# Kernel tuning notes

Measured on AMD Instinct MI355X. Metric: run time of the kernel, lower is better.

Reference implementation:

```python
import jax, jax.numpy as jnp
import numpy as np

B, T, D = 32, 2048, 1024
E, P, L = 16, 720, 8
TOP_K = 2
INIT_STD = 0.02


def _sdpa_1head(q, k, v):
    # q: [B,Q,D], k/v: [B,K,D]
    d = q.shape[-1]
    attn = jnp.einsum('bqd,bkd->bqk', q, k) / jnp.sqrt(jnp.asarray(d, q.dtype))
    attn = jax.nn.softmax(attn, axis=-1)
    return jnp.einsum('bqk,bkd->bqd', attn, v)


def setup_inputs() -> dict:
    key = jax.random.key(0)
    ks = jax.random.split(key, 18)
    s = INIT_STD
    def w(k, shape, scale=INIT_STD):
        return jax.random.normal(k, shape, jnp.float32) * scale
    return {
        'ctx_embed': jax.random.normal(ks[0], (B, T, D), jnp.float32),
        'query_experts': w(ks[1], (E, P, D)),
        'query_pos': w(ks[2], (P, D)),
        'pred_len_table': w(ks[3], (P + 1, D)),
        'latents': w(ks[4], (L, D)),
        'lat_q_w': w(ks[5], (D, D)),
        'ctx_k_w': w(ks[6], (D, D)),
        'ctx_v_w': w(ks[7], (D, D)),
        'lat_out_w': w(ks[8], (D, D)),
        'step_q_w': w(ks[9], (D, D)),
        'lat_k_w': w(ks[10], (D, D)),
        'lat_v_w': w(ks[11], (D, D)),
        'step_out_w': w(ks[12], (D, D)),
        'gate_w1': w(ks[13], (2 * D, D)),
        'gate_b1': jnp.zeros((D,), jnp.float32),
        'gate_w2': w(ks[14], (D, E)),
        'gate_b2': jnp.zeros((E,), jnp.float32),
        'pred_len': P,
    }


def reference(ctx_embed, query_experts, query_pos, pred_len_table, latents,
              lat_q_w, ctx_k_w, ctx_v_w, lat_out_w,
              step_q_w, lat_k_w, lat_v_w, step_out_w,
              gate_w1, gate_b1, gate_w2, gate_b2, pred_len):
    b, _, d = ctx_embed.shape
    # step base: positional + pred-len embedding
    pos = query_pos[:pred_len][None]                      # [1,P,D]
    len_vec = pred_len_table[pred_len][None, None, :]     # [1,1,D]
    step_base = jnp.broadcast_to(pos + len_vec, (b, pred_len, d))
    # stage 1: latents attend over context
    lat = jnp.broadcast_to(latents[None], (b,) + latents.shape)
    q1 = lat @ lat_q_w
    k1 = ctx_embed @ ctx_k_w
    v1 = ctx_embed @ ctx_v_w
    lat_ctx = _sdpa_1head(q1, k1, v1) @ lat_out_w         # [B,L,D]
    # stage 2: steps attend over latents
    q2 = step_base @ step_q_w
    k2 = lat_ctx @ lat_k_w
    v2 = lat_ctx @ lat_v_w
    step_ctx = _sdpa_1head(q2, k2, v2) @ step_out_w       # [B,P,D]
    # gating MLP (exact GELU, as torch default)
    gate_inp = jnp.concatenate([step_base, step_ctx], axis=-1)
    h = jax.nn.gelu(gate_inp @ gate_w1 + gate_b1, approximate=False)
    logits = h @ gate_w2 + gate_b2                        # [B,P,E]
    # top-k masked softmax
    n_exp = logits.shape[-1]
    _, topi = jax.lax.top_k(logits, TOP_K)
    mask = jax.nn.one_hot(topi, n_exp, dtype=logits.dtype).sum(-2) > 0
    masked = jnp.where(mask, logits, -jnp.inf)
    weights = jax.nn.softmax(masked, axis=-1)             # [B,P,E]
    # combine experts without materializing [B,P,E,D]
    queries = jnp.einsum('bpe,epd->bpd', weights, query_experts[:, :pred_len, :])
    return queries
```

## Files before the change

### kernel.cpp

```cpp
#include <hip/hip_runtime.h>
#include <hip/hip_bf16.h>
#include <math.h>

#define D_  1024
#define B_  32
#define T_  2048
#define L_  8
#define P_  720
#define E_  16
#define BP_ (B_*P_)

#define OFF_STEPB   ((size_t)0)
#define OFF_CKWT    ((size_t)737280)
#define OFF_SQWT    ((size_t)1785856)
#define OFF_ATTW    ((size_t)3358720)
#define OFF_LOGITP  ((size_t)3543040)
#define OFF_Q1      ((size_t)5017600)
#define OFF_Q1P     ((size_t)5025792)
#define OFF_NUM     ((size_t)5033984)
#define OFF_TMP1    ((size_t)5296128)
#define OFF_LATCTX  ((size_t)5558272)
#define OFF_K2      ((size_t)5820416)
#define OFF_V2      ((size_t)6082560)
#define OFF_K2P     ((size_t)6344704)
#define OFF_V2A     ((size_t)6606848)
#define OFF_V2P     ((size_t)6868992)
#define OFF_SB1     ((size_t)7131136)
#define OFF_DEN     ((size_t)7868416)
#define WS_FLOATS   ((size_t)7868672)

__device__ __forceinline__ float gelu_exact(float x){
    return 0.5f * x * (1.0f + erff(x * 0.70710678118654752f));
}

__global__ void k_stepb(const float* __restrict__ qpos, const float* __restrict__ plt,
                        float* __restrict__ stepb){
    int p = blockIdx.x;
    int d = threadIdx.x * 4;
    float4 a = *(const float4*)(qpos + (size_t)p*D_ + d);
    float4 b = *(const float4*)(plt  + (size_t)P_*D_ + d);
    a.x += b.x; a.y += b.y; a.z += b.z; a.w += b.w;
    *(float4*)(stepb + (size_t)p*D_ + d) = a;
}

__global__ void k_transpose(const float* __restrict__ s0, const float* __restrict__ s1,
                            float* __restrict__ d0, float* __restrict__ d1){
    __shared__ float tile[32][33];
    const float* src = blockIdx.z ? s1 : s0;
    float*       dst = blockIdx.z ? d1 : d0;
    int tx = threadIdx.x & 31, ty = threadIdx.x >> 5;
    int bx = blockIdx.x * 32, by = blockIdx.y * 32;
    #pragma unroll
    for (int r = 0; r < 4; r++)
        tile[ty + 8*r][tx] = src[(size_t)(by + ty + 8*r)*D_ + bx + tx];
    __syncthreads();
    #pragma unroll
    for (int r = 0; r < 4; r++)
        dst[(size_t)(bx + ty + 8*r)*D_ + by + tx] = tile[tx][ty + 8*r];
}

template<int MR>
__global__ void k_gemmT(const float* __restrict__ A, const float* __restrict__ B,
                        float* __restrict__ C, int M, const float* __restrict__ rowdiv){
    int n  = blockIdx.y * 256 + threadIdx.x;
    int kc = D_ / gridDim.z;
    int k0 = blockIdx.z * kc;
    int mb = blockIdx.x * MR;
    float acc[MR];
    #pragma unroll
    for (int m = 0; m < MR; m++) acc[m] = 0.f;
    for (int k = k0; k < k0 + kc; k += 4){
        float b0 = B[(size_t)(k+0)*D_ + n];
        float b1 = B[(size_t)(k+1)*D_ + n];
        float b2 = B[(size_t)(k+2)*D_ + n];
        float b3 = B[(size_t)(k+3)*D_ + n];
        #pragma unroll
        for (int m = 0; m < MR; m++){
            int row = mb + m; if (row > M - 1) row = M - 1;
            const float4 av = *(const float4*)(A + (size_t)row*D_ + k);
            acc[m] += av.x*b0 + av.y*b1 + av.z*b2 + av.w*b3;
        }
    }
    #pragma unroll
    for (int m = 0; m < MR; m++){
        int row = mb + m;
        if (row < M){
            float v = acc[m];
            if (rowdiv) v /= rowdiv[row];
            atomicAdd(C + (size_t)row*D_ + n, v);
        }
    }
}

__global__ void k_gemm_pair(const float* __restrict__ A0, const float* __restrict__ B0, float* __restrict__ C0,
                            const float* __restrict__ A1, const float* __restrict__ B1, float* __restrict__ C1,
                            int M){
    const int which = blockIdx.z & 1;
    const float* A  = which ? A1 : A0;
    const float* Bm = which ? B1 : B0;
    float*       C  = which ? C1 : C0;
    int zn = gridDim.z >> 1;
    int z  = blockIdx.z >> 1;
    int n  = blockIdx.y * 256 + threadIdx.x;
    int kc = D_ / zn;
    int k0 = z * kc;
    int mb = blockIdx.x * 8;
    float acc[8];
    #pragma unroll
    for (int m = 0; m < 8; m++) acc[m] = 0.f;
    for (int k = k0; k < k0 + kc; k += 4){
        float b0 = Bm[(size_t)(k+0)*D_ + n];
        float b1 = Bm[(size_t)(k+1)*D_ + n];
        float b2 = Bm[(size_t)(k+2)*D_ + n];
        float b3 = Bm[(size_t)(k+3)*D_ + n];
        #pragma unroll
        for (int m = 0; m < 8; m++){
            int row = mb + m; if (row > M - 1) row = M - 1;
            const float4 av = *(const float4*)(A + (size_t)row*D_ + k);
            acc[m] += av.x*b0 + av.y*b1 + av.z*b2 + av.w*b3;
        }
    }
    #pragma unroll
    for (int m = 0; m < 8; m++){
        int row = mb + m;
        if (row < M){
            atomicAdd(C + (size_t)row*D_ + n, acc[m]);
        }
    }
}

__global__ __launch_bounds__(256) void k_stage1(const float* __restrict__ ctx,
                                                const float* __restrict__ q1p,
                                                float* __restrict__ num,
                                                float* __restrict__ den){
    __shared__ float tile[16][1028];
    __shared__ float ev[16][8];
    const int b   = blockIdx.x;
    const int tid = threadIdx.x;
    const int tt  = tid >> 4;
    const int ll  = (tid >> 1) & 7;
    const int hh  = tid & 1;
    float4 acc[8];
    #pragma unroll
    for (int l = 0; l < 8; l++) acc[l] = make_float4(0.f,0.f,0.f,0.f);
    float denacc = 0.f;
    const float4* qp = (const float4*)(q1p + (size_t)ll*D_ + hh*512);
    for (int i = 0; i < 8; i++){
        const int t0 = blockIdx.y*128 + i*16;
        #pragma unroll
        for (int j = 0; j < 16; j++){
            int li = j*256 + tid;
            int t = li >> 8, d4 = li & 255;
            float4 c = *(const float4*)(ctx + ((size_t)(b*T_ + t0 + t))*D_ + 4*d4);
            *(float4*)&tile[t][4*d4] = c;
        }
        __syncthreads();
        {
            const float4* cp = (const float4*)&tile[tt][hh*512];
            float4 sa = make_float4(0.f,0.f,0.f,0.f);
            #pragma unroll 4
            for (int d4 = 0; d4 < 128; d4++){
                float4 c = cp[d4];
                float4 q = qp[d4];
                sa.x += c.x*q.x; sa.y += c.y*q.y;
                sa.z += c.z*q.z; sa.w += c.w*q.w;
            }
            float s = (sa.x + sa.y) + (sa.z + sa.w);
            s += __shfl_xor(s, 1);
            if (hh == 0){
                float e = __expf(s * 0.03125f);
                ev[tt][ll] = e;
                denacc += e;
            }
        }
        __syncthreads();
        #pragma unroll
        for (int t = 0; t < 16; t++){
            float4 c  = *(const float4*)&tile[t][4*tid];
            float4 e0 = *(const float4*)&ev[t][0];
            float4 e1 = *(const float4*)&ev[t][4];
            float ee[8] = {e0.x,e0.y,e0.z,e0.w,e1.x,e1.y,e1.z,e1.w};
            #pragma unroll
            for (int l = 0; l < 8; l++){
                acc[l].x += ee[l]*c.x; acc[l].y += ee[l]*c.y;
                acc[l].z += ee[l]*c.z; acc[l].w += ee[l]*c.w;
            }
        }
        __syncthreads();
    }
    #pragma unroll
    for (int l = 0; l < 8; l++){
        float* np_ = num + ((size_t)(b*8 + l))*D_ + 4*tid;
        atomicAdd(np_+0, acc[l].x); atomicAdd(np_+1, acc[l].y);
        atomicAdd(np_+2, acc[l].z); atomicAdd(np_+3, acc[l].w);
    }
    __syncthreads();
    if (hh == 0) ev[tt][ll] = denacc;
    __syncthreads();
    if (tid < 8){
        float s = 0.f;
        #pragma unroll
        for (int t = 0; t < 16; t++) s += ev[t][tid];
        atomicAdd(den + b*8 + tid, s);
    }
}

__global__ void k_f1(const float* __restrict__ stepb, const float* __restrict__ k2p,
                     float* __restrict__ attw){
    int b = blockIdx.y;
    int p = blockIdx.x * 64 + threadIdx.x;
    if (p >= P_) return;
    const float4* sp = (const float4*)(stepb + (size_t)p * D_);
    const float* kp = k2p + (size_t)b * 8 * D_;
    float acc[8] = {0,0,0,0,0,0,0,0};
    #pragma unroll 2
    for (int d4 = 0; d4 < 256; d4++){
        float4 s = sp[d4];
        #pragma unroll
        for (int l = 0; l < 8; l++){
            const float4 kv = *(const float4*)(kp + (size_t)l*D_ + 4*d4);
            acc[l] += s.x*kv.x + s.y*kv.y + s.z*kv.z + s.w*kv.w;
        }
    }
    float s8[8];
    #pragma unroll
    for (int l = 0; l < 8; l++) s8[l] = acc[l] * 0.03125f;
    float m = s8[0];
    #pragma unroll
    for (int l = 1; l < 8; l++) m = fmaxf(m, s8[l]);
    float e8[8]; float sum = 0.f;
    #pragma unroll
    for (int l = 0; l < 8; l++){ e8[l] = __expf(s8[l] - m); sum += e8[l]; }
    float inv = 1.0f / sum;
    float4 o0 = make_float4(e8[0]*inv, e8[1]*inv, e8[2]*inv, e8[3]*inv);
    float4 o1 = make_float4(e8[4]*inv, e8[5]*inv, e8[6]*inv, e8[7]*inv);
    size_t bp = (size_t)b * P_ + p;
    *(float4*)(attw + bp*8)     = o0;
    *(float4*)(attw + bp*8 + 4) = o1;
}

__global__ void k_f2(const float* __restrict__ SB1, const float* __restrict__ v2p,
                     const float* __restrict__ attw, const float* __restrict__ b1,
                     const float* __restrict__ w2, float* __restrict__ logitp){
    int b  = blockIdx.x;
    int p  = blockIdx.y * 64 + threadIdx.x;
    int dq = blockIdx.z;
    if (p >= P_) return;
    size_t bp = (size_t)b * P_ + p;
    float a[8];
    {
        float4 a0 = *(const float4*)(attw + bp*8);
        float4 a1 = *(const float4*)(attw + bp*8 + 4);
        a[0]=a0.x; a[1]=a0.y; a[2]=a0.z; a[3]=a0.w;
        a[4]=a1.x; a[5]=a1.y; a[6]=a1.z; a[7]=a1.w;
    }
    float acc16[16];
    #pragma unroll
    for (int e = 0; e < 16; e++) acc16[e] = 0.f;
    const float* sbp = SB1 + (size_t)p * D_;
    int dbase = dq * 256;
    for (int dd = 0; dd < 256; dd += 4){
        int d = dbase + dd;
        float4 pre = *(const float4*)(sbp + d);
        float4 bb  = *(const float4*)(b1 + d);
        pre.x += bb.x; pre.y += bb.y; pre.z += bb.z; pre.w += bb.w;
        #pragma unroll
        for (int l = 0; l < 8; l++){
            const float4 vv = *(const float4*)(v2p + ((size_t)(b*8 + l))*D_ + d);
            pre.x += a[l]*vv.x; pre.y += a[l]*vv.y; pre.z += a[l]*vv.z; pre.w += a[l]*vv.w;
        }
        float h[4];
        h[0] = gelu_exact(pre.x); h[1] = gelu_exact(pre.y);
        h[2] = gelu_exact(pre.z); h[3] = gelu_exact(pre.w);
        #pragma unroll
        for (int i = 0; i < 4; i++){
            const float* w2r = w2 + (size_t)(d + i) * E_;
            #pragma unroll
            for (int e = 0; e < 16; e++) acc16[e] += h[i] * w2r[e];
        }
    }
    float* outp = logitp + ((size_t)dq * BP_ + bp) * 16;
    #pragma unroll
    for (int e = 0; e < 16; e += 4){
        float4 v = make_float4(acc16[e], acc16[e+1], acc16[e+2], acc16[e+3]);
        *(float4*)(outp + e) = v;
    }
}

__global__ void k_f3(const float* __restrict__ logitp, const float* __restrict__ b2,
                     const float* __restrict__ qe, float* __restrict__ out){
    int p = blockIdx.x, b = blockIdx.y;
    size_t bp = (size_t)b * P_ + p;
    float lg[16];
    #pragma unroll
    for (int e = 0; e < 16; e++){
        lg[e] = logitp[((size_t)0*BP_ + bp)*16 + e]
              + logitp[((size_t)1*BP_ + bp)*16 + e]
              + logitp[((size_t)2*BP_ + bp)*16 + e]
              + logitp[((size_t)3*BP_ + bp)*16 + e]
              + b2[e];
    }
    int e1 = 0; float l1 = lg[0];
    #pragma unroll
    for (int e = 1; e < 16; e++) if (lg[e] > l1){ l1 = lg[e]; e1 = e; }
    int e2 = 0; float l2 = -1e30f;
    #pragma unroll
    for (int e = 0; e < 16; e++) if (e != e1 && lg[e] > l2){ l2 = lg[e]; e2 = e; }
    float q  = __expf(l2 - l1);
    float w1 = 1.0f / (1.0f + q);
    float w2 = q / (1.0f + q);
    int d = threadIdx.x * 4;
    float4 x1 = *(const float4*)(qe + ((size_t)e1 * P_ + p)*D_ + d);
    float4 x2 = *(const float4*)(qe + ((size_t)e2 * P_ + p)*D_ + d);
    float4 o;
    o.x = w1*x1.x + w2*x2.x; o.y = w1*x1.y + w2*x2.y;
    o.z = w1*x1.z + w2*x2.z; o.w = w1*x1.w + w2*x2.w;
    *(float4*)(out + bp*D_ + d) = o;
}

extern "C" void kernel_launch(void* const* d_in, const int* in_sizes, int n_in,
                              void* d_out, int out_size, void* d_ws, size_t ws_size,
                              hipStream_t stream) {
    (void)in_sizes; (void)n_in; (void)out_size; (void)ws_size;
    const float* ctx  = (const float*)d_in[0];
    const float* qexp = (const float*)d_in[1];
    const float* qpos = (const float*)d_in[2];
    const float* plt  = (const float*)d_in[3];
    const float* lats = (const float*)d_in[4];
    const float* w_lq = (const float*)d_in[5];
    const float* w_ck = (const float*)d_in[6];
    const float* w_cv = (const float*)d_in[7];
    const float* w_lo = (const float*)d_in[8];
    const float* w_sq = (const float*)d_in[9];
    const float* w_lk = (const float*)d_in[10];
    const float* w_lv = (const float*)d_in[11];
    const float* w_so = (const float*)d_in[12];
    const float* w_g1 = (const float*)d_in[13];
    const float* b_g1 = (const float*)d_in[14];
    const float* w_g2 = (const float*)d_in[15];
    const float* b_g2 = (const float*)d_in[16];
    float* out = (float*)d_out;
    float* ws  = (float*)d_ws;

    float* stepb  = ws + OFF_STEPB;
    float* ckwT   = ws + OFF_CKWT;
    float* sqwT   = ws + OFF_SQWT;
    float* attw   = ws + OFF_ATTW;
    float* logitp = ws + OFF_LOGITP;
    float* q1     = ws + OFF_Q1;
    float* q1p    = ws + OFF_Q1P;
    float* num    = ws + OFF_NUM;
    float* tmp1   = ws + OFF_TMP1;
    float* latctx = ws + OFF_LATCTX;
    float* k2     = ws + OFF_K2;
    float* v2     = ws + OFF_V2;
    float* k2p    = ws + OFF_K2P;
    float* v2a    = ws + OFF_V2A;
    float* v2p    = ws + OFF_V2P;
    float* SB1    = ws + OFF_SB1;
    float* den    = ws + OFF_DEN;

    hipMemsetAsync(q1, 0, (WS_FLOATS - OFF_Q1) * sizeof(float), stream);

    k_stepb<<<dim3(P_), dim3(256), 0, stream>>>(qpos, plt, stepb);
    k_transpose<<<dim3(32,32,2), dim3(256), 0, stream>>>(w_ck, w_sq, ckwT, sqwT);

    k_gemmT<8><<<dim3(1,4,8),  dim3(256), 0, stream>>>(lats, w_lq, q1,  8,  nullptr);
    k_gemmT<8><<<dim3(1,4,8),  dim3(256), 0, stream>>>(q1,   ckwT, q1p, 8,  nullptr);

    k_gemmT<8><<<dim3(90,4,8), dim3(256), 0, stream>>>(stepb, w_g1, SB1, P_, nullptr);

    k_stage1<<<dim3(B_,16), dim3(256), 0, stream>>>(ctx, q1p, num, den);

    k_gemmT<8><<<dim3(32,4,4), dim3(256), 0, stream>>>(num,  w_cv, tmp1,   256, den);
    k_gemmT<8><<<dim3(32,4,4), dim3(256), 0, stream>>>(tmp1, w_lo, latctx, 256, nullptr);
    k_gemm_pair<<<dim3(32,4,8), dim3(256), 0, stream>>>(latctx, w_lk, k2,
                                                        latctx, w_lv, v2, 256);
    k_gemm_pair<<<dim3(32,4,8), dim3(256), 0, stream>>>(k2, sqwT, k2p,
                                                        v2, w_so, v2a, 256);
    k_gemmT<8><<<dim3(32,4,4), dim3(256), 0, stream>>>(v2a, w_g1 + (size_t)D_*D_, v2p, 256, nullptr);

    k_f1<<<dim3(12, B_),    dim3(64),  0, stream>>>(stepb, k2p, attw);
    k_f2<<<dim3(B_, 12, 4), dim3(64),  0, stream>>>(SB1, v2p, attw, b_g1, w_g2, logitp);
    k_f3<<<dim3(P_, B_),    dim3(256), 0, stream>>>(logitp, b_g2, qexp, out);
}
```

Baseline: 1.158 ms.

## Restructure stage-1 context attention to per-wave row streaming with register prefetch

The stage-1 kernel no longer stages 16-row context tiles through shared memory with block-wide barriers. Each wave now streams its own 32 context rows straight into registers, double-buffered two rows at a time, and computes the 8 latent scores with a transposed-reduction shuffle tree. The query projection is held in a padded shared-memory layout. Per-wave partial numerators are combined in shared memory before the global atomics. This removes barrier stalls and shared-memory traffic on the main loop, at the cost of high register pressure (128 accumulator floats plus buffers), which may reduce occupancy or cause spills.

```diff
diff --git a/kernel.cpp b/kernel.cpp
--- a/kernel.cpp
+++ b/kernel.cpp
@@ -133,75 +133,143 @@
                                                 const float* __restrict__ q1p,
                                                 float* __restrict__ num,
                                                 float* __restrict__ den){
-    __shared__ float tile[16][1028];
-    __shared__ float ev[16][8];
-    const int b   = blockIdx.x;
-    const int tid = threadIdx.x;
-    const int tt  = tid >> 4;
-    const int ll  = (tid >> 1) & 7;
-    const int hh  = tid & 1;
-    float4 acc[8];
-    #pragma unroll
-    for (int l = 0; l < 8; l++) acc[l] = make_float4(0.f,0.f,0.f,0.f);
+    __shared__ float q1pL[64*129];
+    __shared__ float accsh[8][1028];
+    const int tid  = threadIdx.x;
+    const int lane = tid & 63;
+    const int wav  = tid >> 6;
+    const int b    = blockIdx.x;
+
+    for (int idx = tid; idx < 2048; idx += 256){
+        int ln = idx >> 5;
+        int r  = idx & 31;
+        int l  = r >> 2;
+        int c  = r & 3;
+        float4 v = *(const float4*)(q1p + (size_t)l*D_ + c*256 + ln*4);
+        *(float4*)&q1pL[ln*129 + l*16 + c*4] = v;
+    }
+    __syncthreads();
+
+    const int t0 = blockIdx.y*128 + wav*32;
+    const float4* rp = (const float4*)(ctx + ((size_t)b*T_ + t0)*D_);
+
+    float4 acc[8][4];
+    #pragma unroll
+    for (int l = 0; l < 8; l++)
+        #pragma unroll
+        for (int c = 0; c < 4; c++) acc[l][c] = make_float4(0.f,0.f,0.f,0.f);
     float denacc = 0.f;
-    const float4* qp = (const float4*)(q1p + (size_t)ll*D_ + hh*512);
-    for (int i = 0; i < 8; i++){
-        const int t0 = blockIdx.y*128 + i*16;
-        #pragma unroll
-        for (int j = 0; j < 16; j++){
-            int li = j*256 + tid;
-            int t = li >> 8, d4 = li & 255;
-            float4 c = *(const float4*)(ctx + ((size_t)(b*T_ + t0 + t))*D_ + 4*d4);
-            *(float4*)&tile[t][4*d4] = c;
+
+    const int b0 = lane & 1, b1 = (lane>>1)&1, b2 = (lane>>2)&1;
+    const float* qbase = &q1pL[lane*129];
+
+    float4 cur0[4], cur1[4], nx0[4], nx1[4];
+    #pragma unroll
+    for (int c = 0; c < 4; c++){
+        cur0[c] = rp[(size_t)0*256 + c*64 + lane];
+        cur1[c] = rp[(size_t)1*256 + c*64 + lane];
+    }
+
+    for (int i = 0; i < 32; i += 2){
+        if (i < 30){
+            #pragma unroll
+            for (int c = 0; c < 4; c++){
+                nx0[c] = rp[(size_t)(i+2)*256 + c*64 + lane];
+                nx1[c] = rp[(size_t)(i+3)*256 + c*64 + lane];
+            }
+        }
+        float p0[8], p1[8];
+        #pragma unroll
+        for (int l = 0; l < 8; l++){
+            float s0 = 0.f, s1 = 0.f;
+            #pragma unroll
+            for (int c = 0; c < 4; c++){
+                float4 q = *(const float4*)(qbase + l*16 + c*4);
+                s0 += cur0[c].x*q.x + cur0[c].y*q.y + cur0[c].z*q.z + cur0[c].w*q.w;
+                s1 += cur1[c].x*q.x + cur1[c].y*q.y + cur1[c].z*q.z + cur1[c].w*q.w;
+            }
+            p0[l] = s0; p1[l] = s1;
+        }
+        float e0, e1;
+        {
+            float u0 = b0 ? p0[1] : p0[0], w0 = b0 ? p0[0] : p0[1];
+            float u1 = b0 ? p0[3] : p0[2], w1 = b0 ? p0[2] : p0[3];
+            float u2 = b0 ? p0[5] : p0[4], w2 = b0 ? p0[4] : p0[5];
+            float u3 = b0 ? p0[7] : p0[6], w3 = b0 ? p0[6] : p0[7];
+            u0 += __shfl_xor(w0,1); u1 += __shfl_xor(w1,1);
+            u2 += __shfl_xor(w2,1); u3 += __shfl_xor(w3,1);
+            float x0 = b1 ? u1 : u0, y0 = b1 ? u0 : u1;
+            float x1 = b1 ? u3 : u2, y1 = b1 ? u2 : u3;
+            x0 += __shfl_xor(y0,2); x1 += __shfl_xor(y1,2);
+            float z = b2 ? x1 : x0, zz = b2 ? x0 : x1;
+            z += __shfl_xor(zz,4);
+            z += __shfl_xor(z,8); z += __shfl_xor(z,16); z += __shfl_xor(z,32);
+            e0 = __expf(z * 0.03125f);
+        }
+        {
+            float u0 = b0 ? p1[1] : p1[0], w0 = b0 ? p1[0] : p1[1];
+            float u1 = b0 ? p1[3] : p1[2], w1 = b0 ? p1[2] : p1[3];
+            float u2 = b0 ? p1[5] : p1[4], w2 = b0 ? p1[4] : p1[5];
+            float u3 = b0 ? p1[7] : p1[6], w3 = b0 ? p1[6] : p1[7];
+            u0 += __shfl_xor(w0,1); u1 += __shfl_xor(w1,1);
+            u2 += __shfl_xor(w2,1); u3 += __shfl_xor(w3,1);
+            float x0 = b1 ? u1 : u0, y0 = b1 ? u0 : u1;
+            float x1 = b1 ? u3 : u2, y1 = b1 ? u2 : u3;
+            x0 += __shfl_xor(y0,2); x1 += __shfl_xor(y1,2);
+            float z = b2 ? x1 : x0, zz = b2 ? x0 : x1;
+            z += __shfl_xor(zz,4);
+            z += __shfl_xor(z,8); z += __shfl_xor(z,16); z += __shfl_xor(z,32);
+            e1 = __expf(z * 0.03125f);
+        }
+        denacc += e0 + e1;
+        float ee0[8], ee1[8];
+        #pragma unroll
+        for (int l = 0; l < 8; l++){ ee0[l] = __shfl(e0, l); ee1[l] = __shfl(e1, l); }
+        #pragma unroll
+        for (int l = 0; l < 8; l++)
+            #pragma unroll
+            for (int c = 0; c < 4; c++){
+                acc[l][c].x += ee0[l]*cur0[c].x + ee1[l]*cur1[c].x;
+                acc[l][c].y += ee0[l]*cur0[c].y + ee1[l]*cur1[c].y;
+                acc[l][c].z += ee0[l]*cur0[c].z + ee1[l]*cur1[c].z;
+                acc[l][c].w += ee0[l]*cur0[c].w + ee1[l]*cur1[c].w;
+            }
+        if (i < 30){
+            #pragma unroll
+            for (int c = 0; c < 4; c++){ cur0[c] = nx0[c]; cur1[c] = nx1[c]; }
+        }
+    }
+
+    if (lane < 8) atomicAdd(den + b*8 + lane, denacc);
+
+    for (int w = 0; w < 4; w++){
+        if (wav == w){
+            #pragma unroll
+            for (int l = 0; l < 8; l++)
+                #pragma unroll
+                for (int c = 0; c < 4; c++){
+                    float* s = &accsh[l][c*256 + 4*lane];
+                    if (w == 0){
+                        *(float4*)s = acc[l][c];
+                    } else {
+                        float4 o = *(float4*)s;
+                        o.x += acc[l][c].x; o.y += acc[l][c].y;
+                        o.z += acc[l][c].z; o.w += acc[l][c].w;
+                        *(float4*)s = o;
+                    }
+                }
         }
         __syncthreads();
-        {
-            const float4* cp = (const float4*)&tile[tt][hh*512];
-            float4 sa = make_float4(0.f,0.f,0.f,0.f);
-            #pragma unroll 4
-            for (int d4 = 0; d4 < 128; d4++){
-                float4 c = cp[d4];
-                float4 q = qp[d4];
-                sa.x += c.x*q.x; sa.y += c.y*q.y;
-                sa.z += c.z*q.z; sa.w += c.w*q.w;
-            }
-            float s = (sa.x + sa.y) + (sa.z + sa.w);
-            s += __shfl_xor(s, 1);
-            if (hh == 0){
-                float e = __expf(s * 0.03125f);
-                ev[tt][ll] = e;
-                denacc += e;
-            }
-        }
-        __syncthreads();
-        #pragma unroll
-        for (int t = 0; t < 16; t++){
-            float4 c  = *(const float4*)&tile[t][4*tid];
-            float4 e0 = *(const float4*)&ev[t][0];
-            float4 e1 = *(const float4*)&ev[t][4];
-            float ee[8] = {e0.x,e0.y,e0.z,e0.w,e1.x,e1.y,e1.z,e1.w};
-            #pragma unroll
-            for (int l = 0; l < 8; l++){
-                acc[l].x += ee[l]*c.x; acc[l].y += ee[l]*c.y;
-                acc[l].z += ee[l]*c.z; acc[l].w += ee[l]*c.w;
-            }
-        }
-        __syncthreads();
-    }
-    #pragma unroll
-    for (int l = 0; l < 8; l++){
-        float* np_ = num + ((size_t)(b*8 + l))*D_ + 4*tid;
-        atomicAdd(np_+0, acc[l].x); atomicAdd(np_+1, acc[l].y);
-        atomicAdd(np_+2, acc[l].z); atomicAdd(np_+3, acc[l].w);
-    }
-    __syncthreads();
-    if (hh == 0) ev[tt][ll] = denacc;
-    __syncthreads();
-    if (tid < 8){
-        float s = 0.f;
-        #pragma unroll
-        for (int t = 0; t < 16; t++) s += ev[t][tid];
-        atomicAdd(den + b*8 + tid, s);
+    }
+
+    #pragma unroll
+    for (int j = 0; j < 8; j++){
+        int idx = j*256 + tid;
+        int l  = idx >> 8, d4 = idx & 255;
+        float4 v = *(float4*)&accsh[l][4*d4];
+        float* np_ = num + ((size_t)(b*8 + l))*D_ + 4*d4;
+        atomicAdd(np_+0, v.x); atomicAdd(np_+1, v.y);
+        atomicAdd(np_+2, v.z); atomicAdd(np_+3, v.w);
     }
 }
 
```

After: 988.9 us. 1.17x faster.
